# Kernel optimization log

Hardware: AMD Instinct MI355X
Metric: run time of the kernel (lower is better)

The kernel has to match this reference:

```python
import jax, jax.numpy as jnp
import numpy as np

N, E = 10000, 320000
H, NH, ED = 128, 8, 32
HD = H // NH
FF = 4 * H


def _layer_norm(x, g, b, eps=1e-5):
    m = jnp.mean(x, axis=-1, keepdims=True)
    v = jnp.mean((x - m) ** 2, axis=-1, keepdims=True)
    return (x - m) / jnp.sqrt(v + eps) * g + b


def setup_inputs() -> dict:
    key = jax.random.key(0)
    ks = jax.random.split(key, 16)
    def p(k, shape, fan_in):
        return jax.random.normal(k, shape, jnp.float32) * (fan_in ** -0.5)
    return {
        "x": jax.random.normal(ks[0], (N, H), jnp.float32),
        "edge_index": jax.random.randint(ks[1], (2, E), 0, N, dtype=jnp.int32).astype(jnp.int64),
        "edge_attr": jax.random.normal(ks[2], (E, ED), jnp.float32),
        "Wq": p(ks[3], (H, H), H), "bq": jnp.zeros((H,), jnp.float32),
        "Wk": p(ks[4], (H, H), H), "bk": jnp.zeros((H,), jnp.float32),
        "Wv": p(ks[5], (H, H), H), "bv": jnp.zeros((H,), jnp.float32),
        "We": p(ks[6], (ED, NH), ED), "be": jnp.zeros((NH,), jnp.float32),
        "Wo": p(ks[7], (H, H), H), "bo": jnp.zeros((H,), jnp.float32),
        "ln1_g": jnp.ones((H,), jnp.float32), "ln1_b": jnp.zeros((H,), jnp.float32),
        "W1": p(ks[8], (H, FF), H), "b1": jnp.zeros((FF,), jnp.float32),
        "W2": p(ks[9], (FF, H), FF), "b2": jnp.zeros((H,), jnp.float32),
        "ln2_g": jnp.ones((H,), jnp.float32), "ln2_b": jnp.zeros((H,), jnp.float32),
    }


def reference(x, edge_index, edge_attr, Wq, bq, Wk, bk, Wv, bv, We, be,
              Wo, bo, ln1_g, ln1_b, W1, b1, W2, b2, ln2_g, ln2_b):
    n = x.shape[0]
    src, dst = edge_index[0], edge_index[1]
    # node projections -> [N, NH, HD]
    q = (x @ Wq + bq).reshape(n, NH, HD)
    k = (x @ Wk + bk).reshape(n, NH, HD)
    v = (x @ Wv + bv).reshape(n, NH, HD)
    # per-edge scores [E, NH] with edge-conditioned bias
    edge_bias = edge_attr @ We + be
    scores = jnp.sum(q[src] * k[dst], axis=-1) / jnp.sqrt(jnp.float32(HD)) + edge_bias
    # scatter-softmax over edges grouped by dst
    mx = jax.ops.segment_max(scores, dst, num_segments=n)
    ex = jnp.exp(scores - mx[dst])
    den = jax.ops.segment_sum(ex, dst, num_segments=n)
    attn = ex / (den[dst] + 1e-8)  # [E, NH]
    # weighted scatter-add of source values
    agg = jax.ops.segment_sum(v[src] * attn[..., None], dst, num_segments=n)  # [N, NH, HD]
    out = agg.reshape(n, H) @ Wo + bo
    x = _layer_norm(x + out, ln1_g, ln1_b)
    h = jax.nn.gelu(x @ W1 + b1, approximate=False) @ W2 + b2
    return _layer_norm(x + h, ln2_g, ln2_b)
```

## Files before the change

kernel.cpp:

```cpp
#include <hip/hip_runtime.h>
#include <hip/hip_bf16.h>

#define HH    128
#define NHEAD 8
#define HDIM  16
#define EDIM  32
#define FFDIM 512
#define BM    16
#define CHUNK 16

__global__ __launch_bounds__(512)
void qkv_kernel(const float* __restrict__ x,
                const float* __restrict__ Wq, const float* __restrict__ bq,
                const float* __restrict__ Wk, const float* __restrict__ bk,
                const float* __restrict__ Wv, const float* __restrict__ bv,
                float* __restrict__ q, float* __restrict__ k, float* __restrict__ v,
                int* __restrict__ cnt, int* __restrict__ cursor)
{
    const int row0 = blockIdx.x * BM;
    const int t  = threadIdx.x;
    const int rg = t >> 7;
    const int c  = t & 127;
    __shared__ float xs[BM * HH];

    if (t < BM)                cnt[row0 + t] = 0;
    else if (t < 2 * BM)       cursor[row0 + (t - BM)] = 0;
    *(float4*)&xs[t * 4] = *(const float4*)&x[(size_t)row0 * HH + t * 4];
    __syncthreads();

    float aq[4] = {0.f, 0.f, 0.f, 0.f};
    float ak[4] = {0.f, 0.f, 0.f, 0.f};
    float av[4] = {0.f, 0.f, 0.f, 0.f};
    for (int i0 = 0; i0 < HH; i0 += 4) {
        float4 xr[4];
        #pragma unroll
        for (int r = 0; r < 4; ++r)
            xr[r] = *(const float4*)&xs[(4 * rg + r) * HH + i0];
        #pragma unroll
        for (int u = 0; u < 4; ++u) {
            float wq = Wq[(i0 + u) * HH + c];
            float wk = Wk[(i0 + u) * HH + c];
            float wv = Wv[(i0 + u) * HH + c];
            #pragma unroll
            for (int r = 0; r < 4; ++r) {
                float xv = ((const float*)&xr[r])[u];
                aq[r] += xv * wq;  ak[r] += xv * wk;  av[r] += xv * wv;
            }
        }
    }
    float bqv = bq[c], bkv = bk[c], bvv = bv[c];
    #pragma unroll
    for (int r = 0; r < 4; ++r) {
        size_t o = (size_t)(row0 + 4 * rg + r) * HH + c;
        q[o] = aq[r] + bqv;
        k[o] = ak[r] + bkv;
        v[o] = av[r] + bvv;
    }
}

__global__ void hist_kernel(const int* __restrict__ ei, int E, int* __restrict__ cnt)
{
    int e = blockIdx.x * 256 + threadIdx.x;
    if (e < E) atomicAdd(&cnt[ei[E + e]], 1);
}

#define SCAN_T 1024
__global__ __launch_bounds__(SCAN_T)
void scan_kernel(const int* __restrict__ cnt, int n, int* __restrict__ rowptr)
{
    __shared__ int part[SCAN_T];
    const int t = threadIdx.x;
    const int per = (n + SCAN_T - 1) / SCAN_T;
    const int beg = t * per;
    const int end = min(beg + per, n);
    int sum = 0;
    for (int i = beg; i < end; ++i) sum += cnt[i];
    part[t] = sum;
    __syncthreads();
    for (int off = 1; off < SCAN_T; off <<= 1) {
        int vv = (t >= off) ? part[t - off] : 0;
        __syncthreads();
        part[t] += vv;
        __syncthreads();
    }
    int base = (t == 0) ? 0 : part[t - 1];
    for (int i = beg; i < end; ++i) { rowptr[i] = base; base += cnt[i]; }
    if (t == SCAN_T - 1) rowptr[n] = base;
}

__global__ __launch_bounds__(256)
void scatter_kernel(const int* __restrict__ ei, int E,
                    const float* __restrict__ ea,
                    const float* __restrict__ We, const float* __restrict__ be,
                    const int* __restrict__ rowptr, int* __restrict__ cursor,
                    int* __restrict__ csr_src, float* __restrict__ csr_eb)
{
    __shared__ float wsh[EDIM * NHEAD];
    __shared__ float bsh[NHEAD];
    const int t = threadIdx.x;
    if (t < EDIM * NHEAD) wsh[t] = We[t];
    if (t < NHEAD) bsh[t] = be[t];
    __syncthreads();
    int e = blockIdx.x * 256 + t;
    if (e >= E) return;
    int src = ei[e], dst = ei[E + e];
    int slot = rowptr[dst] + atomicAdd(&cursor[dst], 1);
    csr_src[slot] = src;
    float eb[NHEAD];
    #pragma unroll
    for (int h = 0; h < NHEAD; ++h) eb[h] = bsh[h];
    const float* eap = ea + (size_t)e * EDIM;
    #pragma unroll
    for (int j0 = 0; j0 < EDIM; j0 += 4) {
        float4 a = *(const float4*)&eap[j0];
        #pragma unroll
        for (int h = 0; h < NHEAD; ++h) {
            eb[h] += a.x * wsh[(j0    ) * NHEAD + h]
                   + a.y * wsh[(j0 + 1) * NHEAD + h]
                   + a.z * wsh[(j0 + 2) * NHEAD + h]
                   + a.w * wsh[(j0 + 3) * NHEAD + h];
        }
    }
    #pragma unroll
    for (int h = 0; h < NHEAD; ++h) csr_eb[(size_t)slot * NHEAD + h] = eb[h];
}

__global__ __launch_bounds__(128)
void edge_kernel(const float* __restrict__ q, const float* __restrict__ k,
                 const float* __restrict__ v,
                 const int* __restrict__ rowptr,
                 const int* __restrict__ csr_src, const float* __restrict__ csr_eb,
                 float* __restrict__ agg)
{
    const int node = blockIdx.x;
    const int t = threadIdx.x;
    const int c = t >> 3, h = t & 7;
    const int f = t, fh = t >> 4;
    __shared__ float ks[HH];
    __shared__ float sraw[CHUNK][NHEAD];
    __shared__ float p[CHUNK][NHEAD];
    __shared__ int   ssrc[CHUNK];
    __shared__ float m[NHEAD], dn[NHEAD], fac[NHEAD];

    ks[t] = k[(size_t)node * HH + t];
    if (t < NHEAD) { m[t] = -3.0e38f; dn[t] = 0.f; }
    const int beg = rowptr[node], end = rowptr[node + 1];
    float acc = 0.f;
    __syncthreads();

    for (int b0 = beg; b0 < end; b0 += CHUNK) {
        const int C = min(CHUNK, end - b0);
        float sc = -3.0e38f;
        if (c < C) {
            int src = csr_src[b0 + c];
            if (h == 0) ssrc[c] = src;
            const float* qp = q + (size_t)src * HH + h * HDIM;
            float d0 = 0.f;
            #pragma unroll
            for (int d = 0; d < HDIM; d += 4) {
                float4 qv = *(const float4*)&qp[d];
                d0 += qv.x * ks[h * HDIM + d]     + qv.y * ks[h * HDIM + d + 1]
                    + qv.z * ks[h * HDIM + d + 2] + qv.w * ks[h * HDIM + d + 3];
            }
            sc = d0 * 0.25f + csr_eb[(size_t)(b0 + c) * NHEAD + h];
        }
        sraw[c][h] = sc;
        __syncthreads();
        if (t < NHEAD) {
            float mo = m[t], mc = -3.0e38f;
            #pragma unroll 4
            for (int cc = 0; cc < CHUNK; ++cc) mc = fmaxf(mc, sraw[cc][t]);
            float mn = fmaxf(mo, mc);
            float fa = __expf(mo - mn);
            float s = 0.f;
            #pragma unroll 4
            for (int cc = 0; cc < CHUNK; ++cc) {
                float pe = __expf(sraw[cc][t] - mn);
                p[cc][t] = pe;  s += pe;
            }
            dn[t] = dn[t] * fa + s;
            m[t] = mn;  fac[t] = fa;
        }
        __syncthreads();
        acc *= fac[fh];
        for (int cc = 0; cc < C; ++cc)
            acc += p[cc][fh] * v[(size_t)ssrc[cc] * HH + f];
        __syncthreads();
    }
    agg[(size_t)node * HH + f] = acc / (dn[fh] + 1e-8f);
}

__global__ __launch_bounds__(512)
void tail_kernel(const float* __restrict__ x, const float* __restrict__ agg,
                 const float* __restrict__ Wo, const float* __restrict__ bo,
                 const float* __restrict__ l1g, const float* __restrict__ l1b,
                 const float* __restrict__ W1, const float* __restrict__ b1,
                 const float* __restrict__ W2, const float* __restrict__ b2,
                 const float* __restrict__ l2g, const float* __restrict__ l2b,
                 float* __restrict__ out)
{
    const int row0 = blockIdx.x * BM;
    const int t  = threadIdx.x;
    const int rg = t >> 7;
    const int c  = t & 127;
    const int wavehalf = (t >> 6) & 1;

    __shared__ float xs[BM * HH];
    __shared__ float hs[BM * FFDIM];
    __shared__ float redS[8][4], redS2[8][4];

    *(float4*)&xs[t * 4] = *(const float4*)&agg[(size_t)row0 * HH + t * 4];
    __syncthreads();

    float y[4] = {0.f, 0.f, 0.f, 0.f};
    for (int i0 = 0; i0 < HH; i0 += 4) {
        float4 ar[4];
        #pragma unroll
        for (int r = 0; r < 4; ++r)
            ar[r] = *(const float4*)&xs[(4 * rg + r) * HH + i0];
        #pragma unroll
        for (int u = 0; u < 4; ++u) {
            float w = Wo[(i0 + u) * HH + c];
            #pragma unroll
            for (int r = 0; r < 4; ++r) y[r] += ((const float*)&ar[r])[u] * w;
        }
    }
    {
        float bov = bo[c];
        #pragma unroll
        for (int r = 0; r < 4; ++r)
            y[r] += bov + x[(size_t)(row0 + 4 * rg + r) * HH + c];
    }

    float s[4], s2[4];
    #pragma unroll
    for (int r = 0; r < 4; ++r) { s[r] = y[r]; s2[r] = y[r] * y[r]; }
    #pragma unroll
    for (int off = 32; off > 0; off >>= 1) {
        #pragma unroll
        for (int r = 0; r < 4; ++r) {
            s[r]  += __shfl_down(s[r],  off);
            s2[r] += __shfl_down(s2[r], off);
        }
    }
    if ((t & 63) == 0) {
        #pragma unroll
        for (int r = 0; r < 4; ++r) {
            redS [rg * 2 + wavehalf][r] = s[r];
            redS2[rg * 2 + wavehalf][r] = s2[r];
        }
    }
    __syncthreads();
    float x1v[4];
    {
        float g1 = l1g[c], bb1 = l1b[c];
        #pragma unroll
        for (int r = 0; r < 4; ++r) {
            float ssum = redS [rg * 2][r] + redS [rg * 2 + 1][r];
            float ssq  = redS2[rg * 2][r] + redS2[rg * 2 + 1][r];
            float mean = ssum * (1.0f / HH);
            float var  = ssq  * (1.0f / HH) - mean * mean;
            x1v[r] = (y[r] - mean) * rsqrtf(var + 1e-5f) * g1 + bb1;
        }
    }
    #pragma unroll
    for (int r = 0; r < 4; ++r) xs[(4 * rg + r) * HH + c] = x1v[r];
    __syncthreads();

    float h[4][4];
    #pragma unroll
    for (int r = 0; r < 4; ++r)
        #pragma unroll
        for (int cc = 0; cc < 4; ++cc) h[r][cc] = 0.f;
    for (int i0 = 0; i0 < HH; i0 += 4) {
        float4 xr[4];
        #pragma unroll
        for (int r = 0; r < 4; ++r)
            xr[r] = *(const float4*)&xs[(4 * rg + r) * HH + i0];
        #pragma unroll
        for (int u = 0; u < 4; ++u) {
            float4 w = *(const float4*)&W1[(size_t)(i0 + u) * FFDIM + 4 * c];
            #pragma unroll
            for (int r = 0; r < 4; ++r) {
                float xv = ((const float*)&xr[r])[u];
                h[r][0] += xv * w.x;  h[r][1] += xv * w.y;
                h[r][2] += xv * w.z;  h[r][3] += xv * w.w;
            }
        }
    }
    {
        float4 b1v = *(const float4*)&b1[4 * c];
        #pragma unroll
        for (int r = 0; r < 4; ++r) {
            float4 hv;
            float a0 = h[r][0] + b1v.x, a1 = h[r][1] + b1v.y;
            float a2 = h[r][2] + b1v.z, a3 = h[r][3] + b1v.w;
            hv.x = 0.5f * a0 * (1.0f + erff(a0 * 0.70710678118f));
            hv.y = 0.5f * a1 * (1.0f + erff(a1 * 0.70710678118f));
            hv.z = 0.5f * a2 * (1.0f + erff(a2 * 0.70710678118f));
            hv.w = 0.5f * a3 * (1.0f + erff(a3 * 0.70710678118f));
            *(float4*)&hs[(4 * rg + r) * FFDIM + 4 * c] = hv;
        }
    }
    __syncthreads();

    float y2[4] = {0.f, 0.f, 0.f, 0.f};
    for (int j0 = 0; j0 < FFDIM; j0 += 4) {
        float4 hr[4];
        #pragma unroll
        for (int r = 0; r < 4; ++r)
            hr[r] = *(const float4*)&hs[(4 * rg + r) * FFDIM + j0];
        #pragma unroll
        for (int u = 0; u < 4; ++u) {
            float w = W2[(size_t)(j0 + u) * HH + c];
            #pragma unroll
            for (int r = 0; r < 4; ++r) y2[r] += ((const float*)&hr[r])[u] * w;
        }
    }
    {
        float b2v = b2[c];
        #pragma unroll
        for (int r = 0; r < 4; ++r) y2[r] += b2v + x1v[r];
    }

    #pragma unroll
    for (int r = 0; r < 4; ++r) { s[r] = y2[r]; s2[r] = y2[r] * y2[r]; }
    #pragma unroll
    for (int off = 32; off > 0; off >>= 1) {
        #pragma unroll
        for (int r = 0; r < 4; ++r) {
            s[r]  += __shfl_down(s[r],  off);
            s2[r] += __shfl_down(s2[r], off);
        }
    }
    if ((t & 63) == 0) {
        #pragma unroll
        for (int r = 0; r < 4; ++r) {
            redS [rg * 2 + wavehalf][r] = s[r];
            redS2[rg * 2 + wavehalf][r] = s2[r];
        }
    }
    __syncthreads();
    {
        float g2 = l2g[c], bb2 = l2b[c];
        #pragma unroll
        for (int r = 0; r < 4; ++r) {
            float ssum = redS [rg * 2][r] + redS [rg * 2 + 1][r];
            float ssq  = redS2[rg * 2][r] + redS2[rg * 2 + 1][r];
            float mean = ssum * (1.0f / HH);
            float var  = ssq  * (1.0f / HH) - mean * mean;
            out[(size_t)(row0 + 4 * rg + r) * HH + c] =
                (y2[r] - mean) * rsqrtf(var + 1e-5f) * g2 + bb2;
        }
    }
}

extern "C" void kernel_launch(void* const* d_in, const int* in_sizes, int n_in,
                              void* d_out, int out_size, void* d_ws, size_t ws_size,
                              hipStream_t stream)
{
    const float* x   = (const float*)d_in[0];
    const int*   ei  = (const int*)d_in[1];
    const float* ea  = (const float*)d_in[2];
    const float* Wq  = (const float*)d_in[3];
    const float* bq  = (const float*)d_in[4];
    const float* Wk  = (const float*)d_in[5];
    const float* bk  = (const float*)d_in[6];
    const float* Wv  = (const float*)d_in[7];
    const float* bv  = (const float*)d_in[8];
    const float* We  = (const float*)d_in[9];
    const float* be  = (const float*)d_in[10];
    const float* Wo  = (const float*)d_in[11];
    const float* bo  = (const float*)d_in[12];
    const float* l1g = (const float*)d_in[13];
    const float* l1b = (const float*)d_in[14];
    const float* W1  = (const float*)d_in[15];
    const float* b1  = (const float*)d_in[16];
    const float* W2  = (const float*)d_in[17];
    const float* b2  = (const float*)d_in[18];
    const float* l2g = (const float*)d_in[19];
    const float* l2b = (const float*)d_in[20];
    float* out = (float*)d_out;

    const int n = in_sizes[0] / HH;
    const int E = in_sizes[1] / 2;

    float* ws      = (float*)d_ws;
    float* q       = ws;
    float* k       = q       + (size_t)n * HH;
    float* v       = k       + (size_t)n * HH;
    float* csr_eb  = v       + (size_t)n * HH;
    float* agg     = csr_eb  + (size_t)E * NHEAD;
    int*   cnt     = (int*)(agg + (size_t)n * HH);
    int*   cursor  = cnt     + n;
    int*   rowptr  = cursor  + n;
    int*   csr_src = rowptr  + (n + 1);

    qkv_kernel<<<n / BM, 512, 0, stream>>>(x, Wq, bq, Wk, bk, Wv, bv,
                                           q, k, v, cnt, cursor);
    hist_kernel<<<(E + 255) / 256, 256, 0, stream>>>(ei, E, cnt);
    scan_kernel<<<1, SCAN_T, 0, stream>>>(cnt, n, rowptr);
    scatter_kernel<<<(E + 255) / 256, 256, 0, stream>>>(ei, E, ea, We, be,
                                                        rowptr, cursor,
                                                        csr_src, csr_eb);
    edge_kernel<<<n, 128, 0, stream>>>(q, k, v, rowptr, csr_src, csr_eb, agg);
    tail_kernel<<<n / BM, 512, 0, stream>>>(x, agg, Wo, bo, l1g, l1b,
                                            W1, b1, W2, b2, l2g, l2b, out);
}
```

Before: 324.1 us.

## Remap tail kernel to one row per 32 threads with float4 columns

The fused Wo/LN1/FFN/LN2 tail kernel is restructured so each group of 32 threads owns one row and each thread owns four contiguous columns (float4). This replaces the old layout of four rows times one column per thread. Layer-norm reductions become 32-lane xor shuffles with no shared-memory partials and fewer barriers. In exchange, each weight element loaded is reused across only one row instead of four, which increases weight traffic per FMA from cache.

```diff
diff --git a/kernel.cpp b/kernel.cpp
--- a/kernel.cpp
+++ b/kernel.cpp
@@ -200,158 +200,124 @@
                  float* __restrict__ out)
 {
     const int row0 = blockIdx.x * BM;
-    const int t  = threadIdx.x;
-    const int rg = t >> 7;
-    const int c  = t & 127;
-    const int wavehalf = (t >> 6) & 1;
+    const int t = threadIdx.x;
+    const int r = t >> 5;
+    const int g = t & 31;
+    const int row = row0 + r;
 
     __shared__ float xs[BM * HH];
     __shared__ float hs[BM * FFDIM];
-    __shared__ float redS[8][4], redS2[8][4];
 
     *(float4*)&xs[t * 4] = *(const float4*)&agg[(size_t)row0 * HH + t * 4];
     __syncthreads();
 
-    float y[4] = {0.f, 0.f, 0.f, 0.f};
+    float4 y = make_float4(0.f, 0.f, 0.f, 0.f);
     for (int i0 = 0; i0 < HH; i0 += 4) {
-        float4 ar[4];
-        #pragma unroll
-        for (int r = 0; r < 4; ++r)
-            ar[r] = *(const float4*)&xs[(4 * rg + r) * HH + i0];
+        float4 av = *(const float4*)&xs[r * HH + i0];
         #pragma unroll
         for (int u = 0; u < 4; ++u) {
-            float w = Wo[(i0 + u) * HH + c];
+            float4 w = *(const float4*)&Wo[(size_t)(i0 + u) * HH + 4 * g];
+            float a = ((const float*)&av)[u];
+            y.x += a * w.x;  y.y += a * w.y;  y.z += a * w.z;  y.w += a * w.w;
+        }
+    }
+    {
+        float4 bov = *(const float4*)&bo[4 * g];
+        float4 xv  = *(const float4*)&x[(size_t)row * HH + 4 * g];
+        y.x += bov.x + xv.x;  y.y += bov.y + xv.y;
+        y.z += bov.z + xv.z;  y.w += bov.w + xv.w;
+    }
+
+    float s  = y.x + y.y + y.z + y.w;
+    float s2 = y.x * y.x + y.y * y.y + y.z * y.z + y.w * y.w;
+    #pragma unroll
+    for (int mask = 16; mask > 0; mask >>= 1) {
+        s  += __shfl_xor(s,  mask);
+        s2 += __shfl_xor(s2, mask);
+    }
+    float mean = s * (1.0f / HH);
+    float var  = s2 * (1.0f / HH) - mean * mean;
+    float rstd = rsqrtf(var + 1e-5f);
+    float4 x1v;
+    {
+        float4 gg = *(const float4*)&l1g[4 * g];
+        float4 bb = *(const float4*)&l1b[4 * g];
+        x1v.x = (y.x - mean) * rstd * gg.x + bb.x;
+        x1v.y = (y.y - mean) * rstd * gg.y + bb.y;
+        x1v.z = (y.z - mean) * rstd * gg.z + bb.z;
+        x1v.w = (y.w - mean) * rstd * gg.w + bb.w;
+    }
+    __syncthreads();
+    *(float4*)&xs[r * HH + 4 * g] = x1v;
+    __syncthreads();
+
+    float4 h4[4];
+    #pragma unroll
+    for (int c4 = 0; c4 < 4; ++c4) h4[c4] = make_float4(0.f, 0.f, 0.f, 0.f);
+    for (int i0 = 0; i0 < HH; i0 += 4) {
+        float4 xv = *(const float4*)&xs[r * HH + i0];
+        #pragma unroll
+        for (int u = 0; u < 4; ++u) {
+            const float* wrow = &W1[(size_t)(i0 + u) * FFDIM + 4 * g];
+            float xu = ((const float*)&xv)[u];
             #pragma unroll
-            for (int r = 0; r < 4; ++r) y[r] += ((const float*)&ar[r])[u] * w;
+            for (int c4 = 0; c4 < 4; ++c4) {
+                float4 w = *(const float4*)&wrow[128 * c4];
+                h4[c4].x += xu * w.x;  h4[c4].y += xu * w.y;
+                h4[c4].z += xu * w.z;  h4[c4].w += xu * w.w;
+            }
+        }
+    }
+    #pragma unroll
+    for (int c4 = 0; c4 < 4; ++c4) {
+        float4 bv = *(const float4*)&b1[4 * g + 128 * c4];
+        float a0 = h4[c4].x + bv.x, a1 = h4[c4].y + bv.y;
+        float a2 = h4[c4].z + bv.z, a3 = h4[c4].w + bv.w;
+        float4 hv;
+        hv.x = 0.5f * a0 * (1.0f + erff(a0 * 0.70710678118f));
+        hv.y = 0.5f * a1 * (1.0f + erff(a1 * 0.70710678118f));
+        hv.z = 0.5f * a2 * (1.0f + erff(a2 * 0.70710678118f));
+        hv.w = 0.5f * a3 * (1.0f + erff(a3 * 0.70710678118f));
+        *(float4*)&hs[r * FFDIM + 4 * g + 128 * c4] = hv;
+    }
+    __syncthreads();
+
+    float4 y2 = make_float4(0.f, 0.f, 0.f, 0.f);
+    for (int j0 = 0; j0 < FFDIM; j0 += 4) {
+        float4 hv = *(const float4*)&hs[r * FFDIM + j0];
+        #pragma unroll
+        for (int u = 0; u < 4; ++u) {
+            float4 w = *(const float4*)&W2[(size_t)(j0 + u) * HH + 4 * g];
+            float hu = ((const float*)&hv)[u];
+            y2.x += hu * w.x;  y2.y += hu * w.y;
+            y2.z += hu * w.z;  y2.w += hu * w.w;
         }
     }
     {
-        float bov = bo[c];
-        #pragma unroll
-        for (int r = 0; r < 4; ++r)
-            y[r] += bov + x[(size_t)(row0 + 4 * rg + r) * HH + c];
-    }
-
-    float s[4], s2[4];
-    #pragma unroll
-    for (int r = 0; r < 4; ++r) { s[r] = y[r]; s2[r] = y[r] * y[r]; }
-    #pragma unroll
-    for (int off = 32; off > 0; off >>= 1) {
-        #pragma unroll
-        for (int r = 0; r < 4; ++r) {
-            s[r]  += __shfl_down(s[r],  off);
-            s2[r] += __shfl_down(s2[r], off);
-        }
-    }
-    if ((t & 63) == 0) {
-        #pragma unroll
-        for (int r = 0; r < 4; ++r) {
-            redS [rg * 2 + wavehalf][r] = s[r];
-            redS2[rg * 2 + wavehalf][r] = s2[r];
-        }
-    }
-    __syncthreads();
-    float x1v[4];
+        float4 bv = *(const float4*)&b2[4 * g];
+        y2.x += bv.x + x1v.x;  y2.y += bv.y + x1v.y;
+        y2.z += bv.z + x1v.z;  y2.w += bv.w + x1v.w;
+    }
+
+    s  = y2.x + y2.y + y2.z + y2.w;
+    s2 = y2.x * y2.x + y2.y * y2.y + y2.z * y2.z + y2.w * y2.w;
+    #pragma unroll
+    for (int mask = 16; mask > 0; mask >>= 1) {
+        s  += __shfl_xor(s,  mask);
+        s2 += __shfl_xor(s2, mask);
+    }
+    mean = s * (1.0f / HH);
+    var  = s2 * (1.0f / HH) - mean * mean;
+    rstd = rsqrtf(var + 1e-5f);
     {
-        float g1 = l1g[c], bb1 = l1b[c];
-        #pragma unroll
-        for (int r = 0; r < 4; ++r) {
-            float ssum = redS [rg * 2][r] + redS [rg * 2 + 1][r];
-            float ssq  = redS2[rg * 2][r] + redS2[rg * 2 + 1][r];
-            float mean = ssum * (1.0f / HH);
-            float var  = ssq  * (1.0f / HH) - mean * mean;
-            x1v[r] = (y[r] - mean) * rsqrtf(var + 1e-5f) * g1 + bb1;
-        }
-    }
-    #pragma unroll
-    for (int r = 0; r < 4; ++r) xs[(4 * rg + r) * HH + c] = x1v[r];
-    __syncthreads();
-
-    float h[4][4];
-    #pragma unroll
-    for (int r = 0; r < 4; ++r)
-        #pragma unroll
-        for (int cc = 0; cc < 4; ++cc) h[r][cc] = 0.f;
-    for (int i0 = 0; i0 < HH; i0 += 4) {
-        float4 xr[4];
-        #pragma unroll
-        for (int r = 0; r < 4; ++r)
-            xr[r] = *(const float4*)&xs[(4 * rg + r) * HH + i0];
-        #pragma unroll
-        for (int u = 0; u < 4; ++u) {
-            float4 w = *(const float4*)&W1[(size_t)(i0 + u) * FFDIM + 4 * c];
-            #pragma unroll
-            for (int r = 0; r < 4; ++r) {
-                float xv = ((const float*)&xr[r])[u];
-                h[r][0] += xv * w.x;  h[r][1] += xv * w.y;
-                h[r][2] += xv * w.z;  h[r][3] += xv * w.w;
-            }
-        }
-    }
-    {
-        float4 b1v = *(const float4*)&b1[4 * c];
-        #pragma unroll
-        for (int r = 0; r < 4; ++r) {
-            float4 hv;
-            float a0 = h[r][0] + b1v.x, a1 = h[r][1] + b1v.y;
-            float a2 = h[r][2] + b1v.z, a3 = h[r][3] + b1v.w;
-            hv.x = 0.5f * a0 * (1.0f + erff(a0 * 0.70710678118f));
-            hv.y = 0.5f * a1 * (1.0f + erff(a1 * 0.70710678118f));
-            hv.z = 0.5f * a2 * (1.0f + erff(a2 * 0.70710678118f));
-            hv.w = 0.5f * a3 * (1.0f + erff(a3 * 0.70710678118f));
-            *(float4*)&hs[(4 * rg + r) * FFDIM + 4 * c] = hv;
-        }
-    }
-    __syncthreads();
-
-    float y2[4] = {0.f, 0.f, 0.f, 0.f};
-    for (int j0 = 0; j0 < FFDIM; j0 += 4) {
-        float4 hr[4];
-        #pragma unroll
-        for (int r = 0; r < 4; ++r)
-            hr[r] = *(const float4*)&hs[(4 * rg + r) * FFDIM + j0];
-        #pragma unroll
-        for (int u = 0; u < 4; ++u) {
-            float w = W2[(size_t)(j0 + u) * HH + c];
-            #pragma unroll
-            for (int r = 0; r < 4; ++r) y2[r] += ((const float*)&hr[r])[u] * w;
-        }
-    }
-    {
-        float b2v = b2[c];
-        #pragma unroll
-        for (int r = 0; r < 4; ++r) y2[r] += b2v + x1v[r];
-    }
-
-    #pragma unroll
-    for (int r = 0; r < 4; ++r) { s[r] = y2[r]; s2[r] = y2[r] * y2[r]; }
-    #pragma unroll
-    for (int off = 32; off > 0; off >>= 1) {
-        #pragma unroll
-        for (int r = 0; r < 4; ++r) {
-            s[r]  += __shfl_down(s[r],  off);
-            s2[r] += __shfl_down(s2[r], off);
-        }
-    }
-    if ((t & 63) == 0) {
-        #pragma unroll
-        for (int r = 0; r < 4; ++r) {
-            redS [rg * 2 + wavehalf][r] = s[r];
-            redS2[rg * 2 + wavehalf][r] = s2[r];
-        }
-    }
-    __syncthreads();
-    {
-        float g2 = l2g[c], bb2 = l2b[c];
-        #pragma unroll
-        for (int r = 0; r < 4; ++r) {
-            float ssum = redS [rg * 2][r] + redS [rg * 2 + 1][r];
-            float ssq  = redS2[rg * 2][r] + redS2[rg * 2 + 1][r];
-            float mean = ssum * (1.0f / HH);
-            float var  = ssq  * (1.0f / HH) - mean * mean;
-            out[(size_t)(row0 + 4 * rg + r) * HH + c] =
-                (y2[r] - mean) * rsqrtf(var + 1e-5f) * g2 + bb2;
-        }
+        float4 gg = *(const float4*)&l2g[4 * g];
+        float4 bb = *(const float4*)&l2b[4 * g];
+        float4 o;
+        o.x = (y2.x - mean) * rstd * gg.x + bb.x;
+        o.y = (y2.y - mean) * rstd * gg.y + bb.y;
+        o.z = (y2.z - mean) * rstd * gg.z + bb.z;
+        o.w = (y2.w - mean) * rstd * gg.w + bb.w;
+        *(float4*)&out[(size_t)row * HH + 4 * g] = o;
     }
 }
 
```

Result: slower. 436.3 us (+34.6%).
